# Performance work log

Measured on AMD Instinct MI355X. Metric: run time of the kernel, lower is better.

The kernel has to match this reference:

```python
import jax, jax.numpy as jnp
import numpy as np
from itertools import product as _prod

B = 2          # batch size
NPB = 4096     # voxels per batch
C = 384        # input_dim
H = 8          # num_heads
OUT = 32       # output_dim (seg classes)
SPATIAL = (32, 256, 256)
POOL_R = np.array([1, 2, 2, 2])    # [1]+query_gs_ratio
COMP_R = np.array([1, 16, 16, 16])  # [1]+compress_ratio


def _coords():
    rng = np.random.default_rng(0)
    rows = []
    for b in range(B):
        cand = np.stack([rng.integers(0, s, 4 * NPB) for s in SPATIAL], 1)
        cand = np.unique(cand, axis=0)
        sel = cand[rng.permutation(len(cand))[:NPB]]
        rows.append(np.concatenate([np.full((NPB, 1), b, np.int64), sel], 1))
    return np.concatenate(rows).astype(np.int32)


def setup_inputs() -> dict:
    idx = _coords()                     # [N,4] unique (b,z,y,x)
    N = idx.shape[0]
    pool_u, pool_inv = np.unique(idx // POOL_R, axis=0, return_inverse=True)
    emb_u, emb_inv = np.unique(idx // COMP_R, axis=0, return_inverse=True)
    # submanifold 3x3x3 neighbor table (same batch), -1 = missing
    lut = {tuple(r): i for i, r in enumerate(idx.tolist())}
    nbr = np.full((N, 27), -1, np.int32)
    rows = idx.tolist()
    for k, (dz, dy, dx) in enumerate(_prod((-1, 0, 1), repeat=3)):
        for i, (b, z, y, x) in enumerate(rows):
            nbr[i, k] = lut.get((b, z + dz, y + dy, x + dx), -1)
    key = jax.random.key(0)
    ks = jax.random.split(key, 12)
    g = lambda k, shp, s: jax.random.normal(k, shp, jnp.float32) * s
    s = 1.0 / float(np.sqrt(C))
    return dict(
        feats=g(ks[0], (N, C), 1.0),
        W_pool=g(ks[1], (C, C), s), b_pool=jnp.zeros((C,), jnp.float32),
        W_emb=g(ks[2], (C, C), s), b_emb=jnp.zeros((C,), jnp.float32),
        Wq=g(ks[3], (C, C), s), bq=jnp.zeros((C,), jnp.float32),
        Wk=g(ks[4], (C, C), s), bk=jnp.zeros((C,), jnp.float32),
        Wv=g(ks[5], (C, C), s), bv=jnp.zeros((C,), jnp.float32),
        Wo=g(ks[6], (C, C), s), bo=jnp.zeros((C,), jnp.float32),
        W_conv=g(ks[7], (27, C, OUT), 1.0 / float(np.sqrt(27 * C))),
        b_conv=jnp.zeros((OUT,), jnp.float32),
        pool_inv=jnp.asarray(pool_inv, jnp.int32),
        pool_coords=jnp.asarray(pool_u, jnp.int32),
        emb_inv=jnp.asarray(emb_inv, jnp.int32),
        emb_coords=jnp.asarray(emb_u, jnp.int32),
        nbr_idx=jnp.asarray(nbr),
        batch_size=B,
    )


def _sine_pe(xyz, d_pos):
    # xyz: [n,3] normalized to [0,1]; PositionEmbeddingCoordsSine (3detr-style)
    cdim = d_pos // xyz.shape[1]
    dim_t = 10000.0 ** (2.0 * (jnp.arange(cdim) // 2).astype(jnp.float32) / cdim)
    emb = (xyz * (2.0 * jnp.pi))[:, :, None] / dim_t          # [n,3,cdim]
    pe = jnp.stack([jnp.sin(emb[..., 0::2]), jnp.cos(emb[..., 1::2])], -1)
    return pe.reshape(xyz.shape[0], -1)                        # [n,d_pos]


def reference(feats, W_pool, b_pool, W_emb, b_emb, Wq, bq, Wk, bk, Wv, bv,
              Wo, bo, W_conv, b_conv, pool_inv, pool_coords, emb_inv,
              emb_coords, nbr_idx, batch_size):
    Mp, Me, Cc = pool_coords.shape[0], emb_coords.shape[0], feats.shape[1]
    hd = Cc // H
    # query path: linear + scatter_max over pool cells
    pool_f = jax.ops.segment_max(feats @ W_pool + b_pool, pool_inv, num_segments=Mp)
    # kv path: linear + scatter_max over compressed cells (coords of argmax rows
    # within a cell all equal the unique cell coord, so mean == unique coord)
    emb_f = jax.ops.segment_max(feats @ W_emb + b_emb, emb_inv, num_segments=Me)
    # per-batch min/max-normalized sine positional encoding on concat(emb,pool)
    emb_xyz = emb_coords[:, 1:].astype(jnp.float32)
    pool_xyz = pool_coords[:, 1:].astype(jnp.float32)
    all_xyz = jnp.concatenate([emb_xyz, pool_xyz], 0)
    bids = jnp.concatenate([emb_coords[:, 0], pool_coords[:, 0]], 0)
    mins = jax.ops.segment_min(all_xyz, bids, num_segments=batch_size)
    maxs = jax.ops.segment_max(all_xyz, bids, num_segments=batch_size)
    norm = (all_xyz - mins[bids]) / (maxs[bids] - mins[bids] + 1e-6)
    pe = _sine_pe(norm, Cc)
    emb_f = emb_f + pe[:Me]
    pool_f = pool_f + pe[Me:]
    # multi-head cross-attention, masked to same-batch pairs
    q = (pool_f @ Wq + bq).reshape(Mp, H, hd)
    k = (emb_f @ Wk + bk).reshape(Me, H, hd)
    v = (emb_f @ Wv + bv).reshape(Me, H, hd)
    scores = jnp.einsum('phd,ehd->hpe', q, k) / jnp.sqrt(jnp.float32(hd))
    same_b = pool_coords[:, 0][None, :, None] == emb_coords[:, 0][None, None, :]
    attn = jax.nn.softmax(jnp.where(same_b, scores, -1e9), axis=-1)
    o = jnp.einsum('hpe,ehd->phd', attn, v).reshape(Mp, Cc) @ Wo + bo
    # broadcast back to voxels + residual
    new_f = feats + o[pool_inv]
    # SubMConv3d seg head: gather 27 neighbors, contract with kernel
    valid = (nbr_idx >= 0)[:, :, None]
    gathered = jnp.where(valid, new_f[jnp.maximum(nbr_idx, 0)], 0.0)  # [N,27,C]
    logits = jnp.einsum('nkc,kco->no', gathered, W_conv) + b_conv
    return logits
```

## Files before the change

kernel.cpp:

```cpp
#include <hip/hip_runtime.h>
#include <hip/hip_bf16.h>
#include <math.h>

#define CDIM 384
#define NHEAD 8
#define HD 48
#define OUTD 32
#define MAXB 16
#define CONVK 10368

typedef __bf16 bf16x8 __attribute__((ext_vector_type(8)));
typedef float f32x4 __attribute__((ext_vector_type(4)));

__device__ __forceinline__ f32x4 mfma16(bf16x8 a, bf16x8 b, f32x4 c) {
  return __builtin_amdgcn_mfma_f32_16x16x32_bf16(a, b, c, 0, 0, 0);
}
__device__ __forceinline__ bf16x8 zero8() {
  bf16x8 z = {(__bf16)0.f, (__bf16)0.f, (__bf16)0.f, (__bf16)0.f,
              (__bf16)0.f, (__bf16)0.f, (__bf16)0.f, (__bf16)0.f};
  return z;
}

__device__ __forceinline__ unsigned enc_f(float f) {
  unsigned u = __float_as_uint(f);
  return (u & 0x80000000u) ? ~u : (u | 0x80000000u);
}
__device__ __forceinline__ float dec_f(unsigned u) {
  unsigned v = (u & 0x80000000u) ? (u ^ 0x80000000u) : ~u;
  return __uint_as_float(v);
}

__global__ void init_small_kernel(int* smin, int* smax, int* eb) {
  int t = threadIdx.x;
  if (t < MAXB * 3) { smin[t] = 0x7fffffff; smax[t] = (int)0x80000000; }
  if (t <= MAXB) eb[t] = 0;
}

__global__ void minmax_kernel(const int* __restrict__ ec, int Me,
                              const int* __restrict__ pc, int Mp,
                              int* smin, int* smax) {
  __shared__ int lmin[MAXB * 3], lmax[MAXB * 3];
  int t = threadIdx.x;
  if (t < MAXB * 3) { lmin[t] = 0x7fffffff; lmax[t] = (int)0x80000000; }
  __syncthreads();
  int i = blockIdx.x * blockDim.x + t;
  int tot = Me + Mp;
  if (i < tot) {
    const int* r = (i < Me) ? (ec + 4 * i) : (pc + 4 * (i - Me));
    int b = r[0];
    #pragma unroll
    for (int d = 0; d < 3; ++d) {
      atomicMin(&lmin[b * 3 + d], r[1 + d]);
      atomicMax(&lmax[b * 3 + d], r[1 + d]);
    }
  }
  __syncthreads();
  if (t < MAXB * 3) {
    if (lmin[t] != 0x7fffffff) atomicMin(&smin[t], lmin[t]);
    if (lmax[t] != (int)0x80000000) atomicMax(&smax[t], lmax[t]);
  }
}

__global__ void ebound_kernel(const int* __restrict__ ec, int Me,
                              const int* __restrict__ bsz, int* eb) {
  int e = blockIdx.x * blockDim.x + threadIdx.x;
  if (e == 0) { eb[0] = 0; eb[bsz[0]] = Me; }
  if (e > 0 && e < Me) {
    int b0 = ec[4 * (e - 1)], b1 = ec[4 * e];
    for (int bb = b0 + 1; bb <= b1; ++bb) eb[bb] = e;
  }
}

__global__ __launch_bounds__(256) void prep_kernel(
    const float* __restrict__ feats, __hip_bfloat16* __restrict__ feats16, int N,
    const float* __restrict__ W_pool, const float* __restrict__ W_emb,
    const float* __restrict__ Wk, const float* __restrict__ Wv,
    const float* __restrict__ Wq, const float* __restrict__ Wo,
    __hip_bfloat16* __restrict__ Wt_pe, __hip_bfloat16* __restrict__ Wt_kv,
    __hip_bfloat16* __restrict__ Wt_q, __hip_bfloat16* __restrict__ Wt_o,
    const float* __restrict__ Wc, __hip_bfloat16* __restrict__ Wct,
    __hip_bfloat16* __restrict__ vt, int Mepad,
    int nbF, int nbW, int nbC) {
  int b = blockIdx.x;
  int t = threadIdx.x;
  if (b < nbF) {
    int v = b * 256 + t;
    if (v < N * 48) {
      float4 a0 = *reinterpret_cast<const float4*>(feats + (size_t)v * 8);
      float4 a1 = *reinterpret_cast<const float4*>(feats + (size_t)v * 8 + 4);
      __hip_bfloat16 tmp[8] = {
        __float2bfloat16(a0.x), __float2bfloat16(a0.y), __float2bfloat16(a0.z), __float2bfloat16(a0.w),
        __float2bfloat16(a1.x), __float2bfloat16(a1.y), __float2bfloat16(a1.z), __float2bfloat16(a1.w)};
      *reinterpret_cast<bf16x8*>(feats16 + (size_t)v * 8) = *reinterpret_cast<const bf16x8*>(tmp);
    }
    return;
  }
  b -= nbF;
  if (b < 6 * nbW) {
    int m = b / nbW;
    int v = (b - m * nbW) * 256 + t;
    if (v >= CDIM * 48) return;
    const float* src;
    __hip_bfloat16* dst;
    switch (m) {
      case 0: src = W_pool; dst = Wt_pe; break;
      case 1: src = W_emb;  dst = Wt_pe + (size_t)CDIM * CDIM; break;
      case 2: src = Wk;     dst = Wt_kv; break;
      case 3: src = Wv;     dst = Wt_kv + (size_t)CDIM * CDIM; break;
      case 4: src = Wq;     dst = Wt_q; break;
      default: src = Wo;    dst = Wt_o; break;
    }
    int n = v / 48, k8 = (v - n * 48) * 8;
    __hip_bfloat16 tmp[8];
    #pragma unroll
    for (int u = 0; u < 8; ++u) tmp[u] = __float2bfloat16(src[(size_t)(k8 + u) * CDIM + n]);
    *reinterpret_cast<bf16x8*>(dst + (size_t)n * CDIM + k8) = *reinterpret_cast<const bf16x8*>(tmp);
    return;
  }
  b -= 6 * nbW;
  if (b < nbC) {
    int v = b * 256 + t;
    if (v >= OUTD * (CONVK / 8)) return;
    int n = v / (CONVK / 8), k8 = (v - n * (CONVK / 8)) * 8;
    __hip_bfloat16 tmp[8];
    #pragma unroll
    for (int u = 0; u < 8; ++u) tmp[u] = __float2bfloat16(Wc[(size_t)(k8 + u) * OUTD + n]);
    *reinterpret_cast<bf16x8*>(Wct + (size_t)n * CONVK + k8) = *reinterpret_cast<const bf16x8*>(tmp);
    return;
  }
  b -= nbC;
  {
    int v = b * 256 + t;
    if (v < NHEAD * Mepad) {
      int h = v / Mepad, e = v - h * Mepad;
      vt[(size_t)(h * 64 + HD) * Mepad + e] = __float2bfloat16(1.0f);
    }
  }
}

__global__ void pe_kernel(const unsigned* __restrict__ encP, const unsigned* __restrict__ encE,
                          __hip_bfloat16* __restrict__ pool16, __hip_bfloat16* __restrict__ emb16,
                          const int* __restrict__ pc, int Mp,
                          const int* __restrict__ ec, int Me,
                          const int* __restrict__ smin, const int* __restrict__ smax) {
  int gid = blockIdx.x * blockDim.x + threadIdx.x;
  int total = (Mp + Me) * CDIM;
  if (gid >= total) return;
  int row = gid / CDIM, c = gid - row * CDIM;
  const int* coords;
  const unsigned* src;
  __hip_bfloat16* dst;
  int lrow;
  if (row < Me) { lrow = row; coords = ec + 4 * row; src = encE; dst = emb16; }
  else { lrow = row - Me; coords = pc + 4 * lrow; src = encP; dst = pool16; }
  int b = coords[0];
  int dim = c >> 7;
  int i = c & 127;
  int j = i >> 1;
  float x = (float)coords[1 + dim];
  float mn = (float)smin[b * 3 + dim];
  float mx = (float)smax[b * 3 + dim];
  float nrm = (x - mn) / (mx - mn + 1e-6f);
  float freq = exp2f(-(float)j * 0.20762050593046014f);
  float arg = nrm * 6.283185307179586f * freq;
  float pe = (i & 1) ? cosf(arg) : sinf(arg);
  float val = dec_f(src[(size_t)lrow * CDIM + c]) + pe;
  dst[(size_t)lrow * CDIM + c] = __float2bfloat16(val);
}

template <int EPI>
__global__ __launch_bounds__(256) void mgemm_kernel(
    const __hip_bfloat16* __restrict__ A, int M,
    const __hip_bfloat16* __restrict__ Wt,
    const float* __restrict__ bias0, const float* __restrict__ bias1,
    void* __restrict__ d0, void* __restrict__ d1,
    const int* __restrict__ inv0, const int* __restrict__ inv1,
    int Mepad) {
  __shared__ __align__(16) __hip_bfloat16 As[128][72];
  __shared__ __align__(16) __hip_bfloat16 Bs[64][72];
  const int m0 = blockIdx.x * 128;
  const int n0 = blockIdx.y * 64;
  const int t = threadIdx.x;
  const int lane = t & 63, w = t >> 6;
  const int wr = w >> 1, wc = w & 1;
  const int lq = lane & 15, lg = lane >> 4;

  f32x4 acc[4][2];
  #pragma unroll
  for (int i = 0; i < 4; ++i) {
    acc[i][0] = (f32x4){0.f, 0.f, 0.f, 0.f};
    acc[i][1] = (f32x4){0.f, 0.f, 0.f, 0.f};
  }
  const int arow = t >> 3;
  const int acol = (t & 7) * 8;

  for (int k0 = 0; k0 < CDIM; k0 += 64) {
    #pragma unroll
    for (int i = 0; i < 4; ++i) {
      int r = arow + i * 32;
      int gr = m0 + r;
      bf16x8 val = zero8();
      if (gr < M) val = *reinterpret_cast<const bf16x8*>(A + (size_t)gr * CDIM + k0 + acol);
      *reinterpret_cast<bf16x8*>(&As[r][acol]) = val;
    }
    #pragma unroll
    for (int i = 0; i < 2; ++i) {
      int r = arow + i * 32;
      bf16x8 val = *reinterpret_cast<const bf16x8*>(Wt + (size_t)(n0 + r) * CDIM + k0 + acol);
      *reinterpret_cast<bf16x8*>(&Bs[r][acol]) = val;
    }
    __syncthreads();
    #pragma unroll
    for (int ks = 0; ks < 2; ++ks) {
      bf16x8 af[4], bfv[2];
      #pragma unroll
      for (int fm = 0; fm < 4; ++fm)
        af[fm] = *reinterpret_cast<const bf16x8*>(&As[wr * 64 + fm * 16 + lq][ks * 32 + lg * 8]);
      #pragma unroll
      for (int fn = 0; fn < 2; ++fn)
        bfv[fn] = *reinterpret_cast<const bf16x8*>(&Bs[wc * 32 + fn * 16 + lq][ks * 32 + lg * 8]);
      #pragma unroll
      for (int fm = 0; fm < 4; ++fm)
        #pragma unroll
        for (int fn = 0; fn < 2; ++fn)
          acc[fm][fn] = mfma16(af[fm], bfv[fn], acc[fm][fn]);
    }
    __syncthreads();
  }

  const bool sec = (n0 >= CDIM);
  const int nb = n0 - (sec ? CDIM : 0) + wc * 32;
  const int nA = nb + lq, nB = nb + 16 + lq;

  if (EPI == 0) {
    const float* bias = sec ? bias1 : bias0;
    unsigned* dst = (unsigned*)(sec ? d1 : d0);
    const int* inv = sec ? inv1 : inv0;
    float bA = bias[nA], bB = bias[nB];
    #pragma unroll
    for (int fm = 0; fm < 4; ++fm)
      #pragma unroll
      for (int j = 0; j < 4; ++j) {
        int r = m0 + wr * 64 + fm * 16 + lg * 4 + j;
        if (r < M) {
          int seg = inv[r];
          atomicMax(&dst[(size_t)seg * CDIM + nA], enc_f(acc[fm][0][j] + bA));
          atomicMax(&dst[(size_t)seg * CDIM + nB], enc_f(acc[fm][1][j] + bB));
        }
      }
  } else if (EPI == 1) {
    float bA = bias0[nA], bB = bias0[nB];
    float* dst = (float*)d0;
    #pragma unroll
    for (int fm = 0; fm < 4; ++fm)
      #pragma unroll
      for (int j = 0; j < 4; ++j) {
        int r = m0 + wr * 64 + fm * 16 + lg * 4 + j;
        if (r < M) {
          dst[(size_t)r * CDIM + nA] = acc[fm][0][j] + bA;
          dst[(size_t)r * CDIM + nB] = acc[fm][1][j] + bB;
        }
      }
  } else if (EPI == 2) {
    const float scale = 0.14433756729740643f;
    float bA = bias0[nA], bB = bias0[nB];
    int hA = nA / HD, dA = nA - hA * HD;
    int hB = nB / HD, dB = nB - hB * HD;
    __hip_bfloat16* dst = (__hip_bfloat16*)d0;
    #pragma unroll
    for (int fm = 0; fm < 4; ++fm)
      #pragma unroll
      for (int j = 0; j < 4; ++j) {
        int r = m0 + wr * 64 + fm * 16 + lg * 4 + j;
        if (r < M) {
          dst[(size_t)r * 512 + hA * 64 + dA] = __float2bfloat16((acc[fm][0][j] + bA) * scale);
          dst[(size_t)r * 512 + hB * 64 + dB] = __float2bfloat16((acc[fm][1][j] + bB) * scale);
        }
      }
  } else {
    if (!sec) {
      float bA = bias0[nA], bB = bias0[nB];
      int hA = nA / HD, dA = nA - hA * HD;
      int hB = nB / HD, dB = nB - hB * HD;
      __hip_bfloat16* dst = (__hip_bfloat16*)d0;
      #pragma unroll
      for (int fm = 0; fm < 4; ++fm)
        #pragma unroll
        for (int j = 0; j < 4; ++j) {
          int r = m0 + wr * 64 + fm * 16 + lg * 4 + j;
          if (r < M) {
            dst[(size_t)r * 512 + hA * 64 + dA] = __float2bfloat16(acc[fm][0][j] + bA);
            dst[(size_t)r * 512 + hB * 64 + dB] = __float2bfloat16(acc[fm][1][j] + bB);
          }
        }
    } else {
      float bA = bias1[nA], bB = bias1[nB];
      int hA = nA / HD, dA = nA - hA * HD;
      int hB = nB / HD, dB = nB - hB * HD;
      __hip_bfloat16* dst = (__hip_bfloat16*)d1;
      #pragma unroll
      for (int fm = 0; fm < 4; ++fm)
        #pragma unroll
        for (int j = 0; j < 4; ++j) {
          int r = m0 + wr * 64 + fm * 16 + lg * 4 + j;
          if (r < M) {
            dst[(size_t)(hA * 64 + dA) * Mepad + r] = __float2bfloat16(acc[fm][0][j] + bA);
            dst[(size_t)(hB * 64 + dB) * Mepad + r] = __float2bfloat16(acc[fm][1][j] + bB);
          }
        }
    }
  }
}

__global__ __launch_bounds__(256) void attn_mfma_kernel(
    const __hip_bfloat16* __restrict__ qb, const __hip_bfloat16* __restrict__ kb,
    const __hip_bfloat16* __restrict__ vt, int Mepad,
    const int* __restrict__ pc, const int* __restrict__ eb,
    int Mp, int Me, __hip_bfloat16* __restrict__ ob) {
  __shared__ __align__(16) __hip_bfloat16 Ks[64][72];
  __shared__ __align__(16) __hip_bfloat16 Vs[64][72];
  __shared__ __align__(16) __hip_bfloat16 pl[4][16][72];
  __shared__ int s_lo[4], s_hi[4];
  const int h = blockIdx.y;
  const int t = threadIdx.x;
  const int wv = t >> 6, lane = t & 63;
  const int lq = lane & 15, lg = lane >> 4;
  const int q0 = blockIdx.x * 64 + wv * 16;

  int lo[4], hi[4];
  #pragma unroll
  for (int r = 0; r < 4; ++r) {
    int q = q0 + lg * 4 + r;
    if (q < Mp) { int b = pc[4 * q]; lo[r] = eb[b]; hi[r] = eb[b + 1]; }
    else { lo[r] = 0x7fffffff; hi[r] = 0; }
  }
  int wlo = min(min(lo[0], lo[1]), min(lo[2], lo[3]));
  int whi = max(max(hi[0], hi[1]), max(hi[2], hi[3]));
  #pragma unroll
  for (int off = 1; off < 64; off <<= 1) {
    wlo = min(wlo, __shfl_xor(wlo, off));
    whi = max(whi, __shfl_xor(whi, off));
  }
  if (lane == 0) { s_lo[wv] = wlo; s_hi[wv] = whi; }
  __syncthreads();
  int blo = min(min(s_lo[0], s_lo[1]), min(s_lo[2], s_lo[3]));
  int bhi = max(max(s_hi[0], s_hi[1]), max(s_hi[2], s_hi[3]));
  blo &= ~63;

  int qrow = min(q0 + lq, Mp - 1);
  const __hip_bfloat16* qp = qb + (size_t)qrow * 512 + h * 64 + lg * 8;
  bf16x8 aq0 = *reinterpret_cast<const bf16x8*>(qp);
  bf16x8 aq1 = *reinterpret_cast<const bf16x8*>(qp + 32);

  const int str = t >> 2;
  const int stc = (t & 3) * 16;
  const __hip_bfloat16* vrow = vt + (size_t)(h * 64 + str) * Mepad + stc;

  f32x4 zero = {0.f, 0.f, 0.f, 0.f};
  f32x4 oacc[4];
  oacc[0] = zero; oacc[1] = zero; oacc[2] = zero; oacc[3] = zero;

  bf16x8 k0, k1, v0, v1;
  auto load_tile = [&](int e0) {
    int er = e0 + str;
    k0 = zero8(); k1 = zero8();
    if (er < Me) {
      const __hip_bfloat16* kp = kb + (size_t)er * 512 + h * 64 + stc;
      k0 = *reinterpret_cast<const bf16x8*>(kp);
      k1 = *reinterpret_cast<const bf16x8*>(kp + 8);
    }
    v0 = *reinterpret_cast<const bf16x8*>(vrow + e0);
    v1 = *reinterpret_cast<const bf16x8*>(vrow + e0 + 8);
  };
  load_tile(blo);

  for (int e0 = blo; e0 < bhi; e0 += 64) {
    __syncthreads();
    *reinterpret_cast<bf16x8*>(&Ks[str][stc]) = k0;
    *reinterpret_cast<bf16x8*>(&Ks[str][stc + 8]) = k1;
    *reinterpret_cast<bf16x8*>(&Vs[str][stc]) = v0;
    *reinterpret_cast<bf16x8*>(&Vs[str][stc + 8]) = v1;
    __syncthreads();
    if (e0 + 64 < bhi) load_tile(e0 + 64);

    f32x4 sf[4];
    #pragma unroll
    for (int s = 0; s < 4; ++s) {
      bf16x8 bk0 = *reinterpret_cast<const bf16x8*>(&Ks[s * 16 + lq][lg * 8]);
      bf16x8 bk1 = *reinterpret_cast<const bf16x8*>(&Ks[s * 16 + lq][32 + lg * 8]);
      f32x4 z = zero;
      z = mfma16(aq0, bk0, z);
      z = mfma16(aq1, bk1, z);
      sf[s] = z;
    }
    #pragma unroll
    for (int s = 0; s < 4; ++s) {
      int e = e0 + s * 16 + lq;
      #pragma unroll
      for (int r = 0; r < 4; ++r) {
        bool m = (e >= lo[r]) && (e < hi[r]);
        float p = m ? __expf(sf[s][r]) : 0.f;
        pl[wv][lg * 4 + r][s * 16 + lq] = __float2bfloat16(p);
      }
    }
    asm volatile("s_waitcnt lgkmcnt(0)" ::: "memory");
    __builtin_amdgcn_sched_barrier(0);
    #pragma unroll
    for (int ks = 0; ks < 2; ++ks) {
      bf16x8 ap = *reinterpret_cast<const bf16x8*>(&pl[wv][lq][ks * 32 + lg * 8]);
      #pragma unroll
      for (int dt = 0; dt < 4; ++dt) {
        bf16x8 bv = *reinterpret_cast<const bf16x8*>(&Vs[dt * 16 + lq][ks * 32 + lg * 8]);
        oacc[dt] = mfma16(ap, bv, oacc[dt]);
      }
    }
  }

  #pragma unroll
  for (int r = 0; r < 4; ++r) {
    float l = __shfl(oacc[3][r], (lane & 48));
    int q = q0 + lg * 4 + r;
    if (q < Mp && l > 0.f) {
      float inv = 1.0f / l;
      __hip_bfloat16* op = ob + (size_t)q * CDIM + h * HD;
      op[lq]      = __float2bfloat16(oacc[0][r] * inv);
      op[16 + lq] = __float2bfloat16(oacc[1][r] * inv);
      op[32 + lq] = __float2bfloat16(oacc[2][r] * inv);
    }
  }
}

__global__ void newf16_kernel(const float* __restrict__ feats, const float* __restrict__ o2,
                              const int* __restrict__ pinv, __hip_bfloat16* __restrict__ nf,
                              int N) {
  int v = blockIdx.x * 256 + threadIdx.x;
  if (v >= N * 48) return;
  int n = v / 48, c8 = (v - n * 48) * 8;
  const float* fp = feats + (size_t)n * CDIM + c8;
  const float* op = o2 + (size_t)pinv[n] * CDIM + c8;
  float4 a0 = *reinterpret_cast<const float4*>(fp);
  float4 a1 = *reinterpret_cast<const float4*>(fp + 4);
  float4 b0 = *reinterpret_cast<const float4*>(op);
  float4 b1 = *reinterpret_cast<const float4*>(op + 4);
  __hip_bfloat16 tmp[8] = {
    __float2bfloat16(a0.x + b0.x), __float2bfloat16(a0.y + b0.y),
    __float2bfloat16(a0.z + b0.z), __float2bfloat16(a0.w + b0.w),
    __float2bfloat16(a1.x + b1.x), __float2bfloat16(a1.y + b1.y),
    __float2bfloat16(a1.z + b1.z), __float2bfloat16(a1.w + b1.w)};
  *reinterpret_cast<bf16x8*>(nf + (size_t)v * 8) = *reinterpret_cast<const bf16x8*>(tmp);
}

__global__ __launch_bounds__(256) void mconv_kernel(
    const __hip_bfloat16* __restrict__ nf, const int* __restrict__ nbr,
    const __hip_bfloat16* __restrict__ Wct, float* __restrict__ outp, int N) {
  __shared__ __align__(16) __hip_bfloat16 As[128][72];
  __shared__ __align__(16) __hip_bfloat16 Bs[32][72];
  __shared__ int jrow[128];
  const int n0 = blockIdx.x * 128;
  const int kg = blockIdx.y;
  const int t = threadIdx.x;
  const int lane = t & 63, w = t >> 6;
  const int lq = lane & 15, lg = lane >> 4;
  f32x4 acc[2][2];
  acc[0][0] = (f32x4){0.f,0.f,0.f,0.f}; acc[0][1] = acc[0][0];
  acc[1][0] = acc[0][0]; acc[1][1] = acc[0][0];
  const int arow = t >> 3, acol = (t & 7) * 8;

  for (int kk = kg * 3; kk < kg * 3 + 3; ++kk) {
    __syncthreads();
    if (t < 128) {
      int n = n0 + t;
      jrow[t] = (n < N) ? nbr[(size_t)n * 27 + kk] : -1;
    }
    __syncthreads();
    for (int c0 = 0; c0 < CDIM; c0 += 64) {
      #pragma unroll
      for (int i = 0; i < 4; ++i) {
        int r = arow + i * 32;
        int j = jrow[r];
        bf16x8 val = zero8();
        if (j >= 0) val = *reinterpret_cast<const bf16x8*>(nf + (size_t)j * CDIM + c0 + acol);
        *reinterpret_cast<bf16x8*>(&As[r][acol]) = val;
      }
      {
        int r = t >> 3;
        bf16x8 val = *reinterpret_cast<const bf16x8*>(Wct + (size_t)r * CONVK + kk * CDIM + c0 + acol);
        *reinterpret_cast<bf16x8*>(&Bs[r][acol]) = val;
      }
      __syncthreads();
      #pragma unroll
      for (int ks = 0; ks < 2; ++ks) {
        bf16x8 af[2], bfv[2];
        #pragma unroll
        for (int fm = 0; fm < 2; ++fm)
          af[fm] = *reinterpret_cast<const bf16x8*>(&As[w * 32 + fm * 16 + lq][ks * 32 + lg * 8]);
        #pragma unroll
        for (int fn = 0; fn < 2; ++fn)
          bfv[fn] = *reinterpret_cast<const bf16x8*>(&Bs[fn * 16 + lq][ks * 32 + lg * 8]);
        #pragma unroll
        for (int fm = 0; fm < 2; ++fm)
          #pragma unroll
          for (int fn = 0; fn < 2; ++fn)
            acc[fm][fn] = mfma16(af[fm], bfv[fn], acc[fm][fn]);
      }
      __syncthreads();
    }
  }
  #pragma unroll
  for (int fm = 0; fm < 2; ++fm)
    #pragma unroll
    for (int j = 0; j < 4; ++j) {
      int r = n0 + w * 32 + fm * 16 + lg * 4 + j;
      if (r < N) {
        #pragma unroll
        for (int fn = 0; fn < 2; ++fn)
          outp[((size_t)kg * N + r) * OUTD + fn * 16 + lq] = acc[fm][fn][j];
      }
    }
}

__global__ void conv_reduce_kernel(const float* __restrict__ outp,
                                   const float* __restrict__ bc,
                                   float* __restrict__ out, int N) {
  int v = blockIdx.x * 256 + threadIdx.x;
  if (v >= N * OUTD) return;
  int oo = v & (OUTD - 1);
  float s = bc[oo];
  #pragma unroll
  for (int kg = 0; kg < 9; ++kg) s += outp[(size_t)kg * N * OUTD + v];
  out[v] = s;
}

extern "C" void kernel_launch(void* const* d_in, const int* in_sizes, int n_in,
                              void* d_out, int out_size, void* d_ws, size_t ws_size,
                              hipStream_t stream) {
  const float* feats  = (const float*)d_in[0];
  const float* W_pool = (const float*)d_in[1];
  const float* b_pool = (const float*)d_in[2];
  const float* W_emb  = (const float*)d_in[3];
  const float* b_emb  = (const float*)d_in[4];
  const float* Wq = (const float*)d_in[5];  const float* bq = (const float*)d_in[6];
  const float* Wk = (const float*)d_in[7];  const float* bk = (const float*)d_in[8];
  const float* Wv = (const float*)d_in[9];  const float* bv = (const float*)d_in[10];
  const float* Wo = (const float*)d_in[11]; const float* bo = (const float*)d_in[12];
  const float* Wc = (const float*)d_in[13]; const float* bc = (const float*)d_in[14];
  const int* pool_inv    = (const int*)d_in[15];
  const int* pool_coords = (const int*)d_in[16];
  const int* emb_inv     = (const int*)d_in[17];
  const int* emb_coords  = (const int*)d_in[18];
  const int* nbr         = (const int*)d_in[19];
  const int* bsz         = (const int*)d_in[20];
  int N  = in_sizes[0] / CDIM;
  int Mp = in_sizes[16] / 4;
  int Me = in_sizes[18] / 4;
  int Mepad = ((Me >> 6) + 2) << 6;

  char* wsb = (char*)d_ws;
  size_t off = 0;
  auto alloc = [&](size_t bytes) { void* p = wsb + off; off += (bytes + 255) & ~(size_t)255; return p; };
  unsigned* encA = (unsigned*)alloc((size_t)Mp * CDIM * 4);
  unsigned* encB = (unsigned*)alloc((size_t)Me * CDIM * 4);
  __hip_bfloat16* vt = (__hip_bfloat16*)alloc((size_t)512 * Mepad * 2);
  size_t zspan1 = off;
  __hip_bfloat16* pool16  = (__hip_bfloat16*)alloc((size_t)Mp * CDIM * 2);
  __hip_bfloat16* emb16   = (__hip_bfloat16*)alloc((size_t)Me * CDIM * 2);
  __hip_bfloat16* feats16 = (__hip_bfloat16*)alloc((size_t)N * CDIM * 2);
  float* o2 = (float*)alloc((size_t)Mp * CDIM * 4 > (size_t)9 * N * OUTD * 4
                                ? (size_t)Mp * CDIM * 4 : (size_t)9 * N * OUTD * 4);
  __hip_bfloat16* Wt_pe = (__hip_bfloat16*)alloc((size_t)768 * CDIM * 2);
  __hip_bfloat16* Wt_kv = (__hip_bfloat16*)alloc((size_t)768 * CDIM * 2);
  __hip_bfloat16* Wt_q  = (__hip_bfloat16*)alloc((size_t)CDIM * CDIM * 2);
  __hip_bfloat16* Wt_o  = (__hip_bfloat16*)alloc((size_t)CDIM * CDIM * 2);
  __hip_bfloat16* Wct   = (__hip_bfloat16*)alloc((size_t)OUTD * CONVK * 2);
  int* smin = (int*)alloc(MAXB * 3 * 4);
  int* smax = (int*)alloc(MAXB * 3 * 4);
  int* eb   = (int*)alloc((MAXB + 1) * 4);

  __hip_bfloat16* q16  = (__hip_bfloat16*)encA;
  __hip_bfloat16* k16  = (__hip_bfloat16*)encB;
  __hip_bfloat16* ob16 = pool16;
  __hip_bfloat16* newf16 = feats16;
  float* outp = o2;

  hipMemsetAsync(wsb, 0, zspan1, stream);
  init_small_kernel<<<1, 64, 0, stream>>>(smin, smax, eb);
  {
    int tot = Me + Mp;
    minmax_kernel<<<(tot + 255) / 256, 256, 0, stream>>>(emb_coords, Me, pool_coords, Mp, smin, smax);
    ebound_kernel<<<(Me + 255) / 256, 256, 0, stream>>>(emb_coords, Me, bsz, eb);
  }
  int nbF = (N * 48 + 255) / 256;
  int nbW = (CDIM * 48 + 255) / 256;
  int nbC = (OUTD * (CONVK / 8) + 255) / 256;
  int nbV = (NHEAD * Mepad + 255) / 256;
  prep_kernel<<<nbF + 6 * nbW + nbC + nbV, 256, 0, stream>>>(
      feats, feats16, N, W_pool, W_emb, Wk, Wv, Wq, Wo,
      Wt_pe, Wt_kv, Wt_q, Wt_o, Wc, Wct, vt, Mepad, nbF, nbW, nbC);

  mgemm_kernel<0><<<dim3((N + 127) / 128, 12), 256, 0, stream>>>(
      feats16, N, Wt_pe, b_pool, b_emb, encA, encB, pool_inv, emb_inv, 0);
  pe_kernel<<<((Mp + Me) * CDIM + 255) / 256, 256, 0, stream>>>(
      encA, encB, pool16, emb16, pool_coords, Mp, emb_coords, Me, smin, smax);

  hipMemsetAsync(encA, 0, (size_t)((char*)encB - (char*)encA) + (size_t)Me * 1024, stream);

  mgemm_kernel<2><<<dim3((Mp + 127) / 128, 6), 256, 0, stream>>>(
      pool16, Mp, Wt_q, bq, nullptr, q16, nullptr, nullptr, nullptr, 0);
  mgemm_kernel<3><<<dim3((Me + 127) / 128, 12), 256, 0, stream>>>(
      emb16, Me, Wt_kv, bk, bv, k16, vt, nullptr, nullptr, Mepad);

  attn_mfma_kernel<<<dim3((Mp + 63) / 64, NHEAD), 256, 0, stream>>>(
      q16, k16, vt, Mepad, pool_coords, eb, Mp, Me, ob16);

  mgemm_kernel<1><<<dim3((Mp + 127) / 128, 6), 256, 0, stream>>>(
      ob16, Mp, Wt_o, bo, nullptr, o2, nullptr, nullptr, nullptr, 0);

  newf16_kernel<<<(N * 48 + 255) / 256, 256, 0, stream>>>(feats, o2, pool_inv, newf16, N);

  mconv_kernel<<<dim3((N + 127) / 128, 9), 256, 0, stream>>>(newf16, nbr, Wct, outp, N);
  conv_reduce_kernel<<<(N * OUTD + 255) / 256, 256, 0, stream>>>(outp, bc, (float*)d_out, N);
}
```

Before: 194.6 us.

## Transpose attention score MFMA, fold log2e into Q scale, skip masking on interior tiles

The score MFMA operands are swapped so each lane holds four consecutive keys for one query, which allows packed 8-byte writes of probabilities to LDS. The log2(e) factor is folded into the Q scale so the kernel can use exp2f. Blocks whose queries share one batch range skip the per-element mask on tiles fully inside that range. The weight-transpose prologue index mapping is also reordered so that adjacent threads read contiguous source elements, giving coalesced loads. All of this adds branching and more reductions at kernel start.

```diff
diff --git a/kernel.cpp b/kernel.cpp
--- a/kernel.cpp
+++ b/kernel.cpp
@@ -110,7 +110,9 @@
       case 4: src = Wq;     dst = Wt_q; break;
       default: src = Wo;    dst = Wt_o; break;
     }
-    int n = v / 48, k8 = (v - n * 48) * 8;
+    int k8i = v / CDIM;
+    int n = v - k8i * CDIM;
+    int k8 = k8i * 8;
     __hip_bfloat16 tmp[8];
     #pragma unroll
     for (int u = 0; u < 8; ++u) tmp[u] = __float2bfloat16(src[(size_t)(k8 + u) * CDIM + n]);
@@ -121,7 +123,9 @@
   if (b < nbC) {
     int v = b * 256 + t;
     if (v >= OUTD * (CONVK / 8)) return;
-    int n = v / (CONVK / 8), k8 = (v - n * (CONVK / 8)) * 8;
+    int k8i = v >> 5;
+    int n = v & 31;
+    int k8 = k8i * 8;
     __hip_bfloat16 tmp[8];
     #pragma unroll
     for (int u = 0; u < 8; ++u) tmp[u] = __float2bfloat16(Wc[(size_t)(k8 + u) * OUTD + n]);
@@ -262,7 +266,7 @@
         }
       }
   } else if (EPI == 2) {
-    const float scale = 0.14433756729740643f;
+    const float scale = 0.2082350914f;
     float bA = bias0[nA], bB = bias0[nB];
     int hA = nA / HD, dA = nA - hA * HD;
     int hB = nB / HD, dB = nB - hB * HD;
@@ -320,35 +324,37 @@
   __shared__ __align__(16) __hip_bfloat16 Ks[64][72];
   __shared__ __align__(16) __hip_bfloat16 Vs[64][72];
   __shared__ __align__(16) __hip_bfloat16 pl[4][16][72];
-  __shared__ int s_lo[4], s_hi[4];
+  __shared__ int sred[16];
   const int h = blockIdx.y;
   const int t = threadIdx.x;
   const int wv = t >> 6, lane = t & 63;
   const int lq = lane & 15, lg = lane >> 4;
   const int q0 = blockIdx.x * 64 + wv * 16;
 
-  int lo[4], hi[4];
+  const int q_l = min(q0 + lq, Mp - 1);
+  const int b_l = pc[4 * q_l];
+  const int lo_q = eb[b_l], hi_q = eb[b_l + 1];
+
+  int lomin = lo_q, lomax = lo_q, himin = hi_q, himax = hi_q;
   #pragma unroll
-  for (int r = 0; r < 4; ++r) {
-    int q = q0 + lg * 4 + r;
-    if (q < Mp) { int b = pc[4 * q]; lo[r] = eb[b]; hi[r] = eb[b + 1]; }
-    else { lo[r] = 0x7fffffff; hi[r] = 0; }
-  }
-  int wlo = min(min(lo[0], lo[1]), min(lo[2], lo[3]));
-  int whi = max(max(hi[0], hi[1]), max(hi[2], hi[3]));
-  #pragma unroll
-  for (int off = 1; off < 64; off <<= 1) {
-    wlo = min(wlo, __shfl_xor(wlo, off));
-    whi = max(whi, __shfl_xor(whi, off));
-  }
-  if (lane == 0) { s_lo[wv] = wlo; s_hi[wv] = whi; }
+  for (int off = 1; off < 16; off <<= 1) {
+    lomin = min(lomin, __shfl_xor(lomin, off));
+    lomax = max(lomax, __shfl_xor(lomax, off));
+    himin = min(himin, __shfl_xor(himin, off));
+    himax = max(himax, __shfl_xor(himax, off));
+  }
+  if (lane == 0) {
+    sred[wv * 4 + 0] = lomin; sred[wv * 4 + 1] = lomax;
+    sred[wv * 4 + 2] = himin; sred[wv * 4 + 3] = himax;
+  }
   __syncthreads();
-  int blo = min(min(s_lo[0], s_lo[1]), min(s_lo[2], s_lo[3]));
-  int bhi = max(max(s_hi[0], s_hi[1]), max(s_hi[2], s_hi[3]));
-  blo &= ~63;
-
-  int qrow = min(q0 + lq, Mp - 1);
-  const __hip_bfloat16* qp = qb + (size_t)qrow * 512 + h * 64 + lg * 8;
+  lomin = min(min(sred[0], sred[4]), min(sred[8], sred[12]));
+  lomax = max(max(sred[1], sred[5]), max(sred[9], sred[13]));
+  himin = min(min(sred[2], sred[6]), min(sred[10], sred[14]));
+  himax = max(max(sred[3], sred[7]), max(sred[11], sred[15]));
+  const bool uniform = (lomin == lomax) && (himin == himax);
+
+  const __hip_bfloat16* qp = qb + (size_t)q_l * 512 + h * 64 + lg * 8;
   bf16x8 aq0 = *reinterpret_cast<const bf16x8*>(qp);
   bf16x8 aq1 = *reinterpret_cast<const bf16x8*>(qp + 32);
 
@@ -372,16 +378,17 @@
     v0 = *reinterpret_cast<const bf16x8*>(vrow + e0);
     v1 = *reinterpret_cast<const bf16x8*>(vrow + e0 + 8);
   };
-  load_tile(blo);
-
-  for (int e0 = blo; e0 < bhi; e0 += 64) {
+  const int e0beg = lomin & ~63;
+  load_tile(e0beg);
+
+  for (int e0 = e0beg; e0 < himax; e0 += 64) {
     __syncthreads();
     *reinterpret_cast<bf16x8*>(&Ks[str][stc]) = k0;
     *reinterpret_cast<bf16x8*>(&Ks[str][stc + 8]) = k1;
     *reinterpret_cast<bf16x8*>(&Vs[str][stc]) = v0;
     *reinterpret_cast<bf16x8*>(&Vs[str][stc + 8]) = v1;
     __syncthreads();
-    if (e0 + 64 < bhi) load_tile(e0 + 64);
+    if (e0 + 64 < himax) load_tile(e0 + 64);
 
     f32x4 sf[4];
     #pragma unroll
@@ -389,18 +396,33 @@
       bf16x8 bk0 = *reinterpret_cast<const bf16x8*>(&Ks[s * 16 + lq][lg * 8]);
       bf16x8 bk1 = *reinterpret_cast<const bf16x8*>(&Ks[s * 16 + lq][32 + lg * 8]);
       f32x4 z = zero;
-      z = mfma16(aq0, bk0, z);
-      z = mfma16(aq1, bk1, z);
+      z = mfma16(bk0, aq0, z);
+      z = mfma16(bk1, aq1, z);
       sf[s] = z;
     }
-    #pragma unroll
-    for (int s = 0; s < 4; ++s) {
-      int e = e0 + s * 16 + lq;
-      #pragma unroll
-      for (int r = 0; r < 4; ++r) {
-        bool m = (e >= lo[r]) && (e < hi[r]);
-        float p = m ? __expf(sf[s][r]) : 0.f;
-        pl[wv][lg * 4 + r][s * 16 + lq] = __float2bfloat16(p);
+    const bool interior = uniform && (e0 >= lomin) && (e0 + 64 <= himin);
+    if (interior) {
+      #pragma unroll
+      for (int s = 0; s < 4; ++s) {
+        __hip_bfloat16 tmp[4];
+        #pragma unroll
+        for (int j = 0; j < 4; ++j) tmp[j] = __float2bfloat16(exp2f(sf[s][j]));
+        *reinterpret_cast<uint2*>(&pl[wv][lq][s * 16 + lg * 4]) =
+            *reinterpret_cast<const uint2*>(tmp);
+      }
+    } else {
+      const int ebase = e0 + lg * 4;
+      #pragma unroll
+      for (int s = 0; s < 4; ++s) {
+        __hip_bfloat16 tmp[4];
+        #pragma unroll
+        for (int j = 0; j < 4; ++j) {
+          int e = ebase + s * 16 + j;
+          float p = (e >= lo_q && e < hi_q) ? exp2f(sf[s][j]) : 0.f;
+          tmp[j] = __float2bfloat16(p);
+        }
+        *reinterpret_cast<uint2*>(&pl[wv][lq][s * 16 + lg * 4]) =
+            *reinterpret_cast<const uint2*>(tmp);
       }
     }
     asm volatile("s_waitcnt lgkmcnt(0)" ::: "memory");
```

Measured after the change: 193.1 us. Within noise of the previous version (-0.8%).
